# Optimization experiments

Hardware: AMD Instinct MI355X
Metric: run time of the kernel (lower is better)

The kernel has to match this reference:

```python
import jax, jax.numpy as jnp
import numpy as np

B, T, D = 4, 4096, 1024


def setup_inputs() -> dict:
    key = jax.random.key(0)
    ks = jax.random.split(key, 10)
    scale = 1.0 / np.sqrt(D)
    x = jax.random.normal(ks[0], (B, T, D), jnp.float32)
    last_x = jnp.zeros((D,), jnp.float32)
    last_num = jnp.zeros((D,), jnp.float32)
    last_den = jnp.zeros((D,), jnp.float32)
    time_decay = jax.random.normal(ks[1], (D,), jnp.float32) * 0.1
    time_first = jax.random.normal(ks[2], (D,), jnp.float32) * 0.1
    time_mix_k = jax.random.uniform(ks[3], (1, 1, D), jnp.float32)
    time_mix_v = jax.random.uniform(ks[4], (1, 1, D), jnp.float32)
    time_mix_r = jax.random.uniform(ks[5], (1, 1, D), jnp.float32)
    Wk = jax.random.normal(ks[6], (D, D), jnp.float32) * scale
    Wv = jax.random.normal(ks[7], (D, D), jnp.float32) * scale
    Wr = jax.random.normal(ks[8], (D, D), jnp.float32) * scale
    Wo = jax.random.normal(ks[9], (D, D), jnp.float32) * scale
    return {"x": x, "last_x": last_x, "last_num": last_num, "last_den": last_den,
            "time_decay": time_decay, "time_first": time_first,
            "time_mix_k": time_mix_k, "time_mix_v": time_mix_v, "time_mix_r": time_mix_r,
            "Wk": Wk, "Wv": Wv, "Wr": Wr, "Wo": Wo}


def reference(x, last_x, last_num, last_den, time_decay, time_first,
              time_mix_k, time_mix_v, time_mix_r, Wk, Wv, Wr, Wo):
    # token-shift lerps against the incoming state (broadcast over B, T)
    k = jnp.einsum('btd,ed->bte', x * time_mix_k + last_x * (1.0 - time_mix_k), Wk)
    v = jnp.einsum('btd,ed->bte', x * time_mix_v + last_x * (1.0 - time_mix_v), Wv)
    r = jnp.einsum('btd,ed->bte', x * time_mix_r + last_x * (1.0 - time_mix_r), Wr)
    # WKV numerics, exactly as the original (no extra stabilization)
    efk = jnp.exp(time_first + k)          # exp(time_first + k), [B,T,D]
    wkv = (last_num + efk * v) / (last_den + efk)
    rwkv = jax.nn.sigmoid(r) * wkv
    decay = jnp.exp(-jnp.exp(time_decay))  # [D]
    ek = jnp.exp(k)
    num = decay * last_num + ek * v
    den = decay * last_den + ek
    out = jnp.einsum('btd,ed->bte', rwkv, Wo)
    return out, x[..., -1, :], num[..., -1, :], den[..., -1, :]
```

## Files before the change

kernel.cpp:

```cpp
#include <hip/hip_runtime.h>
#include <cstdint>
#include <cstddef>

constexpr int DD = 1024;
constexpr int TT = 4096;
constexpr int BB = 4;
constexpr int MM = BB * TT;

typedef __bf16 bf16x8 __attribute__((ext_vector_type(8)));
typedef float  f32x4  __attribute__((ext_vector_type(4)));

__device__ __forceinline__ unsigned short f2bf(float f) {
  union { float f; uint32_t u; } c; c.f = f;
  uint32_t r = (c.u + 0x7FFFu + ((c.u >> 16) & 1u)) >> 16;
  return (unsigned short)r;
}

__device__ __forceinline__ float fast_rcp(float x) {
  return __builtin_amdgcn_rcpf(x);
}

__device__ __forceinline__ void async_ld16(const unsigned short* g, unsigned short* lds_dst) {
  __builtin_amdgcn_global_load_lds(
      (const __attribute__((address_space(1))) void*)g,
      (__attribute__((address_space(3))) void*)lds_dst,
      16, 0, 0);
}

__global__ void prep_all(const float* __restrict__ Wk, const float* __restrict__ Wv,
                         const float* __restrict__ Wr, const float* __restrict__ Wo,
                         const float* __restrict__ tmk, const float* __restrict__ tmv,
                         const float* __restrict__ tmr,
                         const float* __restrict__ last_x,
                         const float4* __restrict__ x,
                         unsigned short* __restrict__ wz,
                         unsigned short* __restrict__ wo,
                         float* __restrict__ bias,
                         ushort4* __restrict__ xb,
                         float4* __restrict__ out_xlast) {
  if (blockIdx.x < 1024) {
    int w = (blockIdx.x * 256 + threadIdx.x) >> 6;
    int lane = threadIdx.x & 63;
    int z = w >> 10;
    int e = w & (DD - 1);
    const float* W  = (z == 0) ? Wk  : (z == 1) ? Wv  : (z == 2) ? Wr : Wo;
    const float* tm = (z == 0) ? tmk : (z == 1) ? tmv : tmr;
    unsigned short* dst = (z < 3) ? (wz + (size_t)z * DD * DD + (size_t)e * DD)
                                  : (wo + (size_t)e * DD);
    float s = 0.f;
#pragma unroll
    for (int j = 0; j < 4; ++j) {
      int d = j * 256 + lane * 4;
      float4 wv4 = *(const float4*)(W + (size_t)e * DD + d);
      if (z < 3) {
        float4 t4 = *(const float4*)(tm + d);
        float4 l4 = *(const float4*)(last_x + d);
        s += l4.x * (1.f - t4.x) * wv4.x + l4.y * (1.f - t4.y) * wv4.y +
             l4.z * (1.f - t4.z) * wv4.z + l4.w * (1.f - t4.w) * wv4.w;
        wv4.x *= t4.x; wv4.y *= t4.y; wv4.z *= t4.z; wv4.w *= t4.w;
      }
      ushort4 o;
      o.x = f2bf(wv4.x); o.y = f2bf(wv4.y); o.z = f2bf(wv4.z); o.w = f2bf(wv4.w);
      *(ushort4*)(dst + d) = o;
    }
    if (z < 3) {
      for (int off = 32; off; off >>= 1) s += __shfl_down(s, off, 64);
      if (lane == 0) bias[z * DD + e] = s;
    }
  } else {
    int i = (blockIdx.x - 1024) * 256 + threadIdx.x;
    float4 v = x[i];
    ushort4 o;
    o.x = f2bf(v.x); o.y = f2bf(v.y); o.z = f2bf(v.z); o.w = f2bf(v.w);
    xb[i] = o;
    int m = i >> 8;
    if ((m & (TT - 1)) == (TT - 1)) {
      int b = m >> 12;
      out_xlast[b * 256 + (i & 255)] = v;
    }
  }
}

__global__ __launch_bounds__(256, 2) void gemm_kvr(
    const unsigned short* __restrict__ A,
    const unsigned short* __restrict__ Wz,
    const float* __restrict__ bias,
    const float* __restrict__ time_first, const float* __restrict__ time_decay,
    const float* __restrict__ last_num, const float* __restrict__ last_den,
    unsigned short* __restrict__ rwkv,
    float* __restrict__ out_num, float* __restrict__ out_den) {
  __shared__ unsigned short lA[2][128 * 32];
  __shared__ unsigned short lB[2][3][64 * 32];
  const int tid  = threadIdx.x;
  const int lane = tid & 63;
  const int wave = tid >> 6;
  const int n0 = blockIdx.x * 64;
  const int m0 = blockIdx.y * 128;
  const int wm = (wave >> 1) * 64;
  const int wn = (wave & 1) * 32;

  f32x4 acc[3][4][2] = {};

  const int fr_row = lane & 15;
  const int fr_kb  = (lane >> 4) * 16;
  const int srow = tid >> 2;
  const int scol = (tid & 3) * 8;

  for (int k0 = 0; k0 < DD; k0 += 64) {
    __syncthreads();
#pragma unroll
    for (int h = 0; h < 2; ++h) {
      int kk = k0 + h * 32;
#pragma unroll
      for (int it = 0; it < 2; ++it) {
        int cc  = it * 256 + tid;
        int row = cc >> 2;
        async_ld16(A + (size_t)(m0 + row) * DD + (kk + scol),
                   lA[h] + (size_t)(it * 256 + wave * 64) * 8);
      }
#pragma unroll
      for (int z = 0; z < 3; ++z) {
        async_ld16(Wz + (size_t)z * DD * DD + (size_t)(n0 + srow) * DD + (kk + scol),
                   lB[h][z] + (size_t)(wave * 64) * 8);
      }
    }
    __syncthreads();

#pragma unroll
    for (int h = 0; h < 2; ++h) {
      bf16x8 af[4], bfr[3][2];
#pragma unroll
      for (int i = 0; i < 4; ++i)
        af[i] = *(const bf16x8*)((const char*)lA[h] + ((wm + i * 16 + fr_row) * 64 + fr_kb));
#pragma unroll
      for (int z = 0; z < 3; ++z)
#pragma unroll
        for (int j = 0; j < 2; ++j)
          bfr[z][j] = *(const bf16x8*)((const char*)lB[h][z] + ((wn + j * 16 + fr_row) * 64 + fr_kb));

#pragma unroll
      for (int mi = 0; mi < 4; ++mi)
#pragma unroll
        for (int z = 0; z < 3; ++z)
#pragma unroll
          for (int ni = 0; ni < 2; ++ni)
            acc[z][mi][ni] = __builtin_amdgcn_mfma_f32_16x16x32_bf16(
                af[mi], bfr[z][ni], acc[z][mi][ni], 0, 0, 0);
    }
  }

  const int crow = (lane >> 4) * 4;
  const int ccol = lane & 15;
#pragma unroll
  for (int ni = 0; ni < 2; ++ni) {
    int gnz = n0 + wn + ni * 16 + ccol;
    float bk = bias[gnz], bv = bias[DD + gnz], br = bias[2 * DD + gnz];
    float tf = time_first[gnz];
    float ln = last_num[gnz], ld = last_den[gnz];
#pragma unroll
    for (int mi = 0; mi < 4; ++mi) {
#pragma unroll
      for (int r = 0; r < 4; ++r) {
        int gm = m0 + wm + mi * 16 + crow + r;
        float kk = acc[0][mi][ni][r] + bk;
        float vv = acc[1][mi][ni][r] + bv;
        float rr = acc[2][mi][ni][r] + br;
        float efk = __expf(tf + kk);
        float wkv = (ln + efk * vv) * fast_rcp(ld + efk);
        float sr  = fast_rcp(1.0f + __expf(-rr));
        rwkv[(size_t)gm * DD + gnz] = f2bf(sr * wkv);
        if ((gm & (TT - 1)) == (TT - 1)) {
          int b = gm >> 12;
          float dec = __expf(-__expf(time_decay[gnz]));
          float ek  = __expf(kk);
          out_num[b * DD + gnz] = dec * ln + ek * vv;
          out_den[b * DD + gnz] = dec * ld + ek;
        }
      }
    }
  }
}

__global__ void gemm_bt128(const unsigned short* __restrict__ A,
                           const unsigned short* __restrict__ Bw,
                           float* __restrict__ Cf,
                           int M, int N, int K) {
  __shared__ unsigned short lA[2][128 * 32];
  __shared__ unsigned short lB[2][128 * 32];
  const int tid  = threadIdx.x;
  const int lane = tid & 63;
  const int wave = tid >> 6;
  const int n0 = blockIdx.x * 128;
  const int m0 = blockIdx.y * 128;
  const int wm = (wave >> 1) * 64;
  const int wn = (wave & 1) * 64;

  f32x4 acc[4][4] = {};
  const int fr_row = lane & 15;
  const int fr_kb  = (lane >> 4) * 16;
  const int scol = (tid & 3) * 8;

  for (int k0 = 0; k0 < K; k0 += 64) {
    __syncthreads();
#pragma unroll
    for (int h = 0; h < 2; ++h) {
      int kk = k0 + h * 32;
#pragma unroll
      for (int it = 0; it < 2; ++it) {
        int cc  = it * 256 + tid;
        int row = cc >> 2;
        async_ld16(A + (size_t)(m0 + row) * K + (kk + scol),
                   lA[h] + (size_t)(it * 256 + wave * 64) * 8);
      }
#pragma unroll
      for (int it = 0; it < 2; ++it) {
        int cc  = it * 256 + tid;
        int row = cc >> 2;
        async_ld16(Bw + (size_t)(n0 + row) * K + (kk + scol),
                   lB[h] + (size_t)(it * 256 + wave * 64) * 8);
      }
    }
    __syncthreads();

#pragma unroll
    for (int h = 0; h < 2; ++h) {
      bf16x8 af[4], bfr[4];
#pragma unroll
      for (int i = 0; i < 4; ++i) {
        af[i]  = *(const bf16x8*)((const char*)lA[h] + ((wm + i * 16 + fr_row) * 64 + fr_kb));
        bfr[i] = *(const bf16x8*)((const char*)lB[h] + ((wn + i * 16 + fr_row) * 64 + fr_kb));
      }
#pragma unroll
      for (int mi = 0; mi < 4; ++mi)
#pragma unroll
        for (int ni = 0; ni < 4; ++ni)
          acc[mi][ni] = __builtin_amdgcn_mfma_f32_16x16x32_bf16(af[mi], bfr[ni], acc[mi][ni], 0, 0, 0);
    }
  }

  const int crow = (lane >> 4) * 4;
  const int ccol = lane & 15;
#pragma unroll
  for (int mi = 0; mi < 4; ++mi) {
#pragma unroll
    for (int ni = 0; ni < 4; ++ni) {
      int gn = n0 + wn + ni * 16 + ccol;
#pragma unroll
      for (int r = 0; r < 4; ++r) {
        int gm = m0 + wm + mi * 16 + crow + r;
        Cf[(size_t)gm * N + gn] = acc[mi][ni][r];
      }
    }
  }
}

extern "C" void kernel_launch(void* const* d_in, const int* in_sizes, int n_in,
                              void* d_out, int out_size, void* d_ws, size_t ws_size,
                              hipStream_t stream) {
  const float* x          = (const float*)d_in[0];
  const float* last_x     = (const float*)d_in[1];
  const float* last_num   = (const float*)d_in[2];
  const float* last_den   = (const float*)d_in[3];
  const float* time_decay = (const float*)d_in[4];
  const float* time_first = (const float*)d_in[5];
  const float* tmk        = (const float*)d_in[6];
  const float* tmv        = (const float*)d_in[7];
  const float* tmr        = (const float*)d_in[8];
  const float* Wk         = (const float*)d_in[9];
  const float* Wv         = (const float*)d_in[10];
  const float* Wr         = (const float*)d_in[11];
  const float* Wo         = (const float*)d_in[12];

  float* out       = (float*)d_out;
  float* out_xlast = out + (size_t)MM * DD;
  float* out_num   = out_xlast + BB * DD;
  float* out_den   = out_num + BB * DD;

  char* ws = (char*)d_ws;
  unsigned short* xb   = (unsigned short*)ws;
  unsigned short* wz   = (unsigned short*)(ws + 33554432);
  unsigned short* wo   = (unsigned short*)(ws + 39845888);
  float*          bias = (float*)(ws + 41943040);
  unsigned short* rwkv = (unsigned short*)(ws + 41955328);

  prep_all<<<1024 + MM * DD / 4 / 256, 256, 0, stream>>>(
      Wk, Wv, Wr, Wo, tmk, tmv, tmr, last_x, (const float4*)x,
      wz, wo, bias, (ushort4*)xb, (float4*)out_xlast);

  gemm_kvr<<<dim3(DD / 64, MM / 128), 256, 0, stream>>>(
      xb, wz, bias, time_first, time_decay, last_num, last_den,
      rwkv, out_num, out_den);

  gemm_bt128<<<dim3(DD / 128, MM / 128), 256, 0, stream>>>(
      rwkv, wo, out, MM, DD, DD);
}
```

Measured before the change: 301.1 us.

## Switch GEMMs to 32x32x16 MFMA with XOR-swizzled LDS layout

Both GEMM kernels now use the 32x32x16 bf16 MFMA instead of the 16x16x32 variant, which cuts the number of LDS fragment loads and MFMA issues per k-step. The async global-to-LDS loads are remapped through an XOR-swizzled slot layout so that 32-row fragment reads avoid bank conflicts. The epilogues are rewritten to match the 32x32 accumulator register layout. The risk is more complex address arithmetic and a possible error in the swizzle or epilogue index mapping.

```diff
diff --git a/kernel.cpp b/kernel.cpp
--- a/kernel.cpp
+++ b/kernel.cpp
@@ -8,7 +8,7 @@
 constexpr int MM = BB * TT;
 
 typedef __bf16 bf16x8 __attribute__((ext_vector_type(8)));
-typedef float  f32x4  __attribute__((ext_vector_type(4)));
+typedef float  f32x16 __attribute__((ext_vector_type(16)));
 
 __device__ __forceinline__ unsigned short f2bf(float f) {
   union { float f; uint32_t u; } c; c.f = f;
@@ -25,6 +25,15 @@
       (const __attribute__((address_space(1))) void*)g,
       (__attribute__((address_space(3))) void*)lds_dst,
       16, 0, 0);
+}
+
+__device__ __forceinline__ int lds_slot(int r, int c) {
+  return ((r >> 1) << 3) + ((((r & 1) << 2) | c) ^ ((r >> 1) & 7));
+}
+__device__ __forceinline__ void slot_decode(int p, int& r, int& c) {
+  int L = p >> 3, u = (p & 7) ^ (L & 7);
+  r = (L << 1) | (u >> 2);
+  c = u & 3;
 }
 
 __global__ void prep_all(const float* __restrict__ Wk, const float* __restrict__ Wv,
@@ -99,28 +108,28 @@
   const int wm = (wave >> 1) * 64;
   const int wn = (wave & 1) * 32;
 
-  f32x4 acc[3][4][2] = {};
-
-  const int fr_row = lane & 15;
-  const int fr_kb  = (lane >> 4) * 16;
-  const int srow = tid >> 2;
-  const int scol = (tid & 3) * 8;
+  f32x16 acc[3][2] = {};
+
+  const int l31 = lane & 31;
+  const int lhi = lane >> 5;
+
+  int srA0, scA0, srA1, scA1, srB, scB;
+  slot_decode(tid,       srA0, scA0);
+  slot_decode(256 + tid, srA1, scA1);
+  slot_decode(tid,       srB,  scB);
 
   for (int k0 = 0; k0 < DD; k0 += 64) {
     __syncthreads();
 #pragma unroll
     for (int h = 0; h < 2; ++h) {
       int kk = k0 + h * 32;
-#pragma unroll
-      for (int it = 0; it < 2; ++it) {
-        int cc  = it * 256 + tid;
-        int row = cc >> 2;
-        async_ld16(A + (size_t)(m0 + row) * DD + (kk + scol),
-                   lA[h] + (size_t)(it * 256 + wave * 64) * 8);
-      }
+      async_ld16(A + (size_t)(m0 + srA0) * DD + (kk + scA0 * 8),
+                 lA[h] + (size_t)(wave * 64) * 8);
+      async_ld16(A + (size_t)(m0 + srA1) * DD + (kk + scA1 * 8),
+                 lA[h] + (size_t)(256 + wave * 64) * 8);
 #pragma unroll
       for (int z = 0; z < 3; ++z) {
-        async_ld16(Wz + (size_t)z * DD * DD + (size_t)(n0 + srow) * DD + (kk + scol),
+        async_ld16(Wz + (size_t)z * DD * DD + (size_t)(n0 + srB) * DD + (kk + scB * 8),
                    lB[h][z] + (size_t)(wave * 64) * 8);
       }
     }
@@ -128,54 +137,50 @@
 
 #pragma unroll
     for (int h = 0; h < 2; ++h) {
-      bf16x8 af[4], bfr[3][2];
-#pragma unroll
-      for (int i = 0; i < 4; ++i)
-        af[i] = *(const bf16x8*)((const char*)lA[h] + ((wm + i * 16 + fr_row) * 64 + fr_kb));
-#pragma unroll
-      for (int z = 0; z < 3; ++z)
-#pragma unroll
-        for (int j = 0; j < 2; ++j)
-          bfr[z][j] = *(const bf16x8*)((const char*)lB[h][z] + ((wn + j * 16 + fr_row) * 64 + fr_kb));
-
-#pragma unroll
-      for (int mi = 0; mi < 4; ++mi)
+#pragma unroll
+      for (int h16 = 0; h16 < 2; ++h16) {
+        int cc = h16 * 2 + lhi;
+        bf16x8 af[2], bz[3];
+#pragma unroll
+        for (int mi = 0; mi < 2; ++mi)
+          af[mi] = *(const bf16x8*)(lA[h] + (size_t)lds_slot(wm + mi * 32 + l31, cc) * 8);
 #pragma unroll
         for (int z = 0; z < 3; ++z)
-#pragma unroll
-          for (int ni = 0; ni < 2; ++ni)
-            acc[z][mi][ni] = __builtin_amdgcn_mfma_f32_16x16x32_bf16(
-                af[mi], bfr[z][ni], acc[z][mi][ni], 0, 0, 0);
-    }
-  }
-
-  const int crow = (lane >> 4) * 4;
-  const int ccol = lane & 15;
-#pragma unroll
-  for (int ni = 0; ni < 2; ++ni) {
-    int gnz = n0 + wn + ni * 16 + ccol;
-    float bk = bias[gnz], bv = bias[DD + gnz], br = bias[2 * DD + gnz];
-    float tf = time_first[gnz];
-    float ln = last_num[gnz], ld = last_den[gnz];
-#pragma unroll
-    for (int mi = 0; mi < 4; ++mi) {
-#pragma unroll
-      for (int r = 0; r < 4; ++r) {
-        int gm = m0 + wm + mi * 16 + crow + r;
-        float kk = acc[0][mi][ni][r] + bk;
-        float vv = acc[1][mi][ni][r] + bv;
-        float rr = acc[2][mi][ni][r] + br;
-        float efk = __expf(tf + kk);
-        float wkv = (ln + efk * vv) * fast_rcp(ld + efk);
-        float sr  = fast_rcp(1.0f + __expf(-rr));
-        rwkv[(size_t)gm * DD + gnz] = f2bf(sr * wkv);
-        if ((gm & (TT - 1)) == (TT - 1)) {
-          int b = gm >> 12;
-          float dec = __expf(-__expf(time_decay[gnz]));
-          float ek  = __expf(kk);
-          out_num[b * DD + gnz] = dec * ln + ek * vv;
-          out_den[b * DD + gnz] = dec * ld + ek;
-        }
+          bz[z] = *(const bf16x8*)(lB[h][z] + (size_t)lds_slot(wn + l31, cc) * 8);
+#pragma unroll
+        for (int z = 0; z < 3; ++z)
+#pragma unroll
+          for (int mi = 0; mi < 2; ++mi)
+            acc[z][mi] = __builtin_amdgcn_mfma_f32_32x32x16_bf16(
+                af[mi], bz[z], acc[z][mi], 0, 0, 0);
+      }
+    }
+  }
+
+  const int gnz = n0 + wn + l31;
+  const float bk = bias[gnz], bv = bias[DD + gnz], br = bias[2 * DD + gnz];
+  const float tf = time_first[gnz];
+  const float ln = last_num[gnz], ld = last_den[gnz];
+  const int rbase = 4 * lhi;
+#pragma unroll
+  for (int mi = 0; mi < 2; ++mi) {
+#pragma unroll
+    for (int reg = 0; reg < 16; ++reg) {
+      int row = (reg & 3) + 8 * (reg >> 2) + rbase;
+      int gm = m0 + wm + mi * 32 + row;
+      float kk = acc[0][mi][reg] + bk;
+      float vv = acc[1][mi][reg] + bv;
+      float rr = acc[2][mi][reg] + br;
+      float efk = __expf(tf + kk);
+      float wkv = (ln + efk * vv) * fast_rcp(ld + efk);
+      float sr  = fast_rcp(1.0f + __expf(-rr));
+      rwkv[(size_t)gm * DD + gnz] = f2bf(sr * wkv);
+      if ((gm & (TT - 1)) == (TT - 1)) {
+        int b = gm >> 12;
+        float dec = __expf(-__expf(time_decay[gnz]));
+        float ek  = __expf(kk);
+        out_num[b * DD + gnz] = dec * ln + ek * vv;
+        out_den[b * DD + gnz] = dec * ld + ek;
       }
     }
   }
@@ -195,60 +200,62 @@
   const int wm = (wave >> 1) * 64;
   const int wn = (wave & 1) * 64;
 
-  f32x4 acc[4][4] = {};
-  const int fr_row = lane & 15;
-  const int fr_kb  = (lane >> 4) * 16;
-  const int scol = (tid & 3) * 8;
+  f32x16 acc[2][2] = {};
+  const int l31 = lane & 31;
+  const int lhi = lane >> 5;
+
+  int sr0, sc0, sr1, sc1;
+  slot_decode(tid,       sr0, sc0);
+  slot_decode(256 + tid, sr1, sc1);
 
   for (int k0 = 0; k0 < K; k0 += 64) {
     __syncthreads();
 #pragma unroll
     for (int h = 0; h < 2; ++h) {
       int kk = k0 + h * 32;
-#pragma unroll
-      for (int it = 0; it < 2; ++it) {
-        int cc  = it * 256 + tid;
-        int row = cc >> 2;
-        async_ld16(A + (size_t)(m0 + row) * K + (kk + scol),
-                   lA[h] + (size_t)(it * 256 + wave * 64) * 8);
-      }
-#pragma unroll
-      for (int it = 0; it < 2; ++it) {
-        int cc  = it * 256 + tid;
-        int row = cc >> 2;
-        async_ld16(Bw + (size_t)(n0 + row) * K + (kk + scol),
-                   lB[h] + (size_t)(it * 256 + wave * 64) * 8);
-      }
+      async_ld16(A + (size_t)(m0 + sr0) * K + (kk + sc0 * 8),
+                 lA[h] + (size_t)(wave * 64) * 8);
+      async_ld16(A + (size_t)(m0 + sr1) * K + (kk + sc1 * 8),
+                 lA[h] + (size_t)(256 + wave * 64) * 8);
+      async_ld16(Bw + (size_t)(n0 + sr0) * K + (kk + sc0 * 8),
+                 lB[h] + (size_t)(wave * 64) * 8);
+      async_ld16(Bw + (size_t)(n0 + sr1) * K + (kk + sc1 * 8),
+                 lB[h] + (size_t)(256 + wave * 64) * 8);
     }
     __syncthreads();
 
 #pragma unroll
     for (int h = 0; h < 2; ++h) {
-      bf16x8 af[4], bfr[4];
-#pragma unroll
-      for (int i = 0; i < 4; ++i) {
-        af[i]  = *(const bf16x8*)((const char*)lA[h] + ((wm + i * 16 + fr_row) * 64 + fr_kb));
-        bfr[i] = *(const bf16x8*)((const char*)lB[h] + ((wn + i * 16 + fr_row) * 64 + fr_kb));
-      }
-#pragma unroll
-      for (int mi = 0; mi < 4; ++mi)
-#pragma unroll
-        for (int ni = 0; ni < 4; ++ni)
-          acc[mi][ni] = __builtin_amdgcn_mfma_f32_16x16x32_bf16(af[mi], bfr[ni], acc[mi][ni], 0, 0, 0);
-    }
-  }
-
-  const int crow = (lane >> 4) * 4;
-  const int ccol = lane & 15;
-#pragma unroll
-  for (int mi = 0; mi < 4; ++mi) {
-#pragma unroll
-    for (int ni = 0; ni < 4; ++ni) {
-      int gn = n0 + wn + ni * 16 + ccol;
-#pragma unroll
-      for (int r = 0; r < 4; ++r) {
-        int gm = m0 + wm + mi * 16 + crow + r;
-        Cf[(size_t)gm * N + gn] = acc[mi][ni][r];
+#pragma unroll
+      for (int h16 = 0; h16 < 2; ++h16) {
+        int cc = h16 * 2 + lhi;
+        bf16x8 af[2], bf[2];
+#pragma unroll
+        for (int i = 0; i < 2; ++i) {
+          af[i] = *(const bf16x8*)(lA[h] + (size_t)lds_slot(wm + i * 32 + l31, cc) * 8);
+          bf[i] = *(const bf16x8*)(lB[h] + (size_t)lds_slot(wn + i * 32 + l31, cc) * 8);
+        }
+#pragma unroll
+        for (int mi = 0; mi < 2; ++mi)
+#pragma unroll
+          for (int ni = 0; ni < 2; ++ni)
+            acc[mi][ni] = __builtin_amdgcn_mfma_f32_32x32x16_bf16(
+                af[mi], bf[ni], acc[mi][ni], 0, 0, 0);
+      }
+    }
+  }
+
+  const int rbase = 4 * lhi;
+#pragma unroll
+  for (int mi = 0; mi < 2; ++mi) {
+#pragma unroll
+    for (int ni = 0; ni < 2; ++ni) {
+      int gn = n0 + wn + ni * 32 + l31;
+#pragma unroll
+      for (int reg = 0; reg < 16; ++reg) {
+        int row = (reg & 3) + 8 * (reg >> 2) + rbase;
+        int gm = m0 + wm + mi * 32 + row;
+        Cf[(size_t)gm * N + gn] = acc[mi][ni][reg];
       }
     }
   }
```

Result: slower. 311.9 us (+3.6%).
